# Optimization experiments

Measured on AMD Instinct MI355X. Metric: run time of the kernel, lower is better.

The kernel has to match this reference:

```python
import jax, jax.numpy as jnp
import numpy as np


def setup_inputs() -> dict:
    key = jax.random.key(0)
    ks = jax.random.split(key, 7)
    B, T, D = 4, 4096, 128
    s = 0.02
    return {
        "input_data": jax.random.normal(ks[0], (B, T, D), dtype=jnp.float32),
        "Wq": jax.random.normal(ks[1], (D, D), dtype=jnp.float32) * s,
        "bq": jax.random.normal(ks[2], (D,), dtype=jnp.float32) * s,
        "Wk": jax.random.normal(ks[3], (D, D), dtype=jnp.float32) * s,
        "bk": jax.random.normal(ks[4], (D,), dtype=jnp.float32) * s,
        "Wv": jax.random.normal(ks[5], (D, D), dtype=jnp.float32) * s,
        "bv": jax.random.normal(ks[6], (D,), dtype=jnp.float32) * s,
    }


def reference(input_data, Wq, bq, Wk, bk, Wv, bv):
    D = input_data.shape[-1]
    scale = jnp.asarray(D, input_data.dtype) ** 0.5
    # torch Linear: x @ W.T + b
    q = input_data @ Wq.T + bq  # [B,T,D]
    k = input_data @ Wk.T + bk
    v = input_data @ Wv.T + bv
    energy = jnp.einsum("btd,bsd->bts", q, k) / scale  # [B,T,T]
    attn = jax.nn.softmax(energy, axis=-1)
    return jnp.einsum("bts,bsd->btd", attn, v)  # [B,T,D]
```

## Files before the change

kernel.cpp:

```cpp
#include <hip/hip_runtime.h>
#include <cstdint>

typedef _Float16 half2_t __attribute__((ext_vector_type(2)));
typedef _Float16 half4_t __attribute__((ext_vector_type(4)));
typedef _Float16 half8_t __attribute__((ext_vector_type(8)));
typedef float floatx4 __attribute__((ext_vector_type(4)));

#define T_SEQ 4096
#define D_HEAD 128
#define SCALE_LOG2 0.12751742526f

__device__ __forceinline__ void gload16(const void* src, void* dst_lds) {
    using gptr_t = const __attribute__((address_space(1))) unsigned int*;
    using lptr_t = __attribute__((address_space(3))) unsigned int*;
    __builtin_amdgcn_global_load_lds((gptr_t)(uintptr_t)src,
                                     (lptr_t)(unsigned int)(uintptr_t)dst_lds, 16, 0, 0);
}

__device__ __forceinline__ float exp2_raw(float x) {
#if __has_builtin(__builtin_amdgcn_exp2f)
    return __builtin_amdgcn_exp2f(x);
#else
    return exp2f(x);
#endif
}

__global__ __launch_bounds__(256) void proj_kernel(
    const float* __restrict__ x,
    const float* __restrict__ Wq, const float* __restrict__ bq,
    const float* __restrict__ Wk, const float* __restrict__ bk,
    const float* __restrict__ Wv, const float* __restrict__ bv,
    _Float16* __restrict__ qf, _Float16* __restrict__ kf, _Float16* __restrict__ vt)
{
    __shared__ __align__(16) _Float16 Ws[128 * 136];
    __shared__ __align__(16) _Float16 xs[64 * 136];

    const int t = threadIdx.x;
    const int mat = blockIdx.y;
    const float* W = (mat == 0) ? Wq : (mat == 1) ? Wk : Wv;
    const float* bias = (mat == 0) ? bq : (mat == 1) ? bk : bv;
    const float osc = (mat == 0) ? SCALE_LOG2 : 1.0f;
    const int r0 = blockIdx.x * 64;

    {
        const int o = t >> 1;
        const int i0 = (t & 1) * 64;
        for (int jj = 0; jj < 8; ++jj) {
            floatx4 w0 = *reinterpret_cast<const floatx4*>(W + o * 128 + i0 + jj * 8);
            floatx4 w1 = *reinterpret_cast<const floatx4*>(W + o * 128 + i0 + jj * 8 + 4);
            half8_t h;
            h[0]=(_Float16)w0[0]; h[1]=(_Float16)w0[1]; h[2]=(_Float16)w0[2]; h[3]=(_Float16)w0[3];
            h[4]=(_Float16)w1[0]; h[5]=(_Float16)w1[1]; h[6]=(_Float16)w1[2]; h[7]=(_Float16)w1[3];
            *reinterpret_cast<half8_t*>(&Ws[o * 136 + i0 + jj * 8]) = h;
        }
    }
    {
        const int row = t >> 2;
        const int c0 = (t & 3) * 32;
        for (int jj = 0; jj < 4; ++jj) {
            floatx4 w0 = *reinterpret_cast<const floatx4*>(x + (size_t)(r0 + row) * 128 + c0 + jj * 8);
            floatx4 w1 = *reinterpret_cast<const floatx4*>(x + (size_t)(r0 + row) * 128 + c0 + jj * 8 + 4);
            half8_t h;
            h[0]=(_Float16)w0[0]; h[1]=(_Float16)w0[1]; h[2]=(_Float16)w0[2]; h[3]=(_Float16)w0[3];
            h[4]=(_Float16)w1[0]; h[5]=(_Float16)w1[1]; h[6]=(_Float16)w1[2]; h[7]=(_Float16)w1[3];
            *reinterpret_cast<half8_t*>(&xs[row * 136 + c0 + jj * 8]) = h;
        }
    }
    __syncthreads();

    const int w = t >> 6;
    const int lane = t & 63;
    const int lo = lane & 15, hi = lane >> 4;

    floatx4 acc[8] = {};
    for (int dc = 0; dc < 4; ++dc) {
        half8_t a8 = *reinterpret_cast<const half8_t*>(&xs[(w * 16 + lo) * 136 + dc * 32 + hi * 8]);
        for (int ot = 0; ot < 8; ++ot) {
            half8_t b8 = *reinterpret_cast<const half8_t*>(&Ws[(ot * 16 + lo) * 136 + dc * 32 + hi * 8]);
            acc[ot] = __builtin_amdgcn_mfma_f32_16x16x32_f16(a8, b8, acc[ot], 0, 0, 0);
        }
    }
    __syncthreads();

    float bb[8];
    for (int ot = 0; ot < 8; ++ot) bb[ot] = bias[ot * 16 + lo];

    if (mat < 2) {
        _Float16* ol = xs;
        for (int ot = 0; ot < 8; ++ot)
            for (int r = 0; r < 4; ++r)
                ol[(w * 16 + hi * 4 + r) * 136 + ot * 16 + lo] = (_Float16)((acc[ot][r] + bb[ot]) * osc);
        __syncthreads();
        _Float16* dst = (mat == 0) ? qf : kf;
        for (int i = 0; i < 4; ++i) {
            int c = t + 256 * i;
            int row = c >> 4, p = c & 15;
            half8_t v = *reinterpret_cast<const half8_t*>(&ol[row * 136 + p * 8]);
            *reinterpret_cast<half8_t*>(dst + (size_t)(r0 + row) * 128 + p * 8) = v;
        }
    } else {
        _Float16* vl = Ws;
        for (int ot = 0; ot < 8; ++ot)
            for (int r = 0; r < 4; ++r)
                vl[(ot * 16 + lo) * 72 + w * 16 + hi * 4 + r] = (_Float16)(acc[ot][r] + bb[ot]);
        __syncthreads();
        const int b = r0 >> 12, tl0 = r0 & 4095;
        for (int i = 0; i < 4; ++i) {
            int c = t + 256 * i;
            int d = c >> 3, p = c & 7;
            half8_t v = *reinterpret_cast<const half8_t*>(&vl[d * 72 + p * 8]);
            *reinterpret_cast<half8_t*>(vt + ((size_t)(b * 128 + d)) * 4096 + tl0 + p * 8) = v;
        }
    }
}

__global__ __launch_bounds__(512, 1) void attn_kernel(
    const _Float16* __restrict__ qf, const _Float16* __restrict__ kf,
    const _Float16* __restrict__ vt, float* __restrict__ out)
{
    __shared__ __align__(16) char smem[100352];

    const int tid = threadIdx.x;
    const int w = tid >> 6, lane = tid & 63;
    const int lo = lane & 15, hi = lane >> 4;
    const int qg = w & 1, ksp = w >> 1;

    const int bx = blockIdx.x;
    const int wg = (bx & 7) * 32 + (bx >> 3);
    const int b = wg >> 6;
    const int q0 = (wg & 63) * 64;

    const char* kbc = (const char*)(kf + (size_t)b * T_SEQ * 128);
    const char* vbc = (const char*)(vt + (size_t)b * 128 * T_SEQ);

    int koff[2], kdst[2];
#pragma unroll
    for (int r = 0; r < 2; ++r) {
        int seg = w * 2 + r;
        int slot = lane & 15;
        int row = seg * 4 + (lane >> 4);
        koff[r] = row * 256 + ((slot ^ (row & 7)) << 4);
        kdst[r] = seg * 1024 + lane * 16;
    }
    int vgo[2], vwl[2];
#pragma unroll
    for (int i = 0; i < 2; ++i) {
        int d = (tid >> 3) + 64 * i;
        vgo[i] = d * (T_SEQ * 2) + (tid & 7) * 16;
        vwl[i] = 16384 + d * 128 + (((tid & 7) ^ (d & 7)) << 4);
    }
    int kro[4];
#pragma unroll
    for (int dc = 0; dc < 4; ++dc)
        kro[dc] = (ksp * 16 + lo) * 256 + (((dc * 4 + hi) ^ (lo & 7)) << 4);
    int vro[8];
#pragma unroll
    for (int dt = 0; dt < 8; ++dt)
        vro[dt] = 16384 + (dt * 16 + lo) * 128 +
                  (((ksp * 2 + (hi >> 1)) ^ (lo & 7)) << 4) + ((hi & 1) << 3);

    half8_t qfA[4], qfB[4];
    {
        const _Float16* qa = qf + ((size_t)b * T_SEQ + q0 + qg * 32 + lo) * 128;
        const _Float16* qb = qa + 16 * 128;
#pragma unroll
        for (int dc = 0; dc < 4; ++dc) {
            qfA[dc] = *reinterpret_cast<const half8_t*>(qa + dc * 32 + hi * 8);
            qfB[dc] = *reinterpret_cast<const half8_t*>(qb + dc * 32 + hi * 8);
        }
    }

    floatx4 accA[8] = {}, accB[8] = {};
    float mA = -1e30f, mB = -1e30f, lA = 0.f, lB = 0.f;
    half4_t paA = {}, paB = {};

    gload16(kbc + koff[0], smem + kdst[0]);
    gload16(kbc + koff[1], smem + kdst[1]);
    {
        uint4 v0 = *reinterpret_cast<const uint4*>(vbc + vgo[0]);
        uint4 v1 = *reinterpret_cast<const uint4*>(vbc + vgo[1]);
        *reinterpret_cast<uint4*>(smem + vwl[0]) = v0;
        *reinterpret_cast<uint4*>(smem + vwl[1]) = v1;
    }
    __syncthreads();

#define TILE(T0, CUR, NXT, PRV, PF, DOPREV) do {                                       \
    uint4 vr0, vr1;                                                                    \
    if (PF) {                                                                          \
        const char* vs = vbc + (size_t)((T0) + 64) * 2;                                \
        vr0 = *reinterpret_cast<const uint4*>(vs + vgo[0]);                            \
        vr1 = *reinterpret_cast<const uint4*>(vs + vgo[1]);                            \
        const char* ks = kbc + (size_t)((T0) + 64) * 256;                              \
        gload16(ks + koff[0], smem + (NXT) + kdst[0]);                                 \
        gload16(ks + koff[1], smem + (NXT) + kdst[1]);                                 \
    }                                                                                  \
    floatx4 sA = {0.f,0.f,0.f,0.f}, sB = {0.f,0.f,0.f,0.f};                            \
    __builtin_amdgcn_s_setprio(1);                                                     \
    _Pragma("unroll")                                                                  \
    for (int dc = 0; dc < 4; ++dc) {                                                   \
        half8_t kf8 = *reinterpret_cast<const half8_t*>(smem + (CUR) + kro[dc]);       \
        sA = __builtin_amdgcn_mfma_f32_16x16x32_f16(kf8, qfA[dc], sA, 0, 0, 0);        \
        sB = __builtin_amdgcn_mfma_f32_16x16x32_f16(kf8, qfB[dc], sB, 0, 0, 0);        \
    }                                                                                  \
    __builtin_amdgcn_s_setprio(0);                                                     \
    float mpA = fmaxf(fmaxf(sA[0], sA[1]), fmaxf(sA[2], sA[3]));                       \
    float mpB = fmaxf(fmaxf(sB[0], sB[1]), fmaxf(sB[2], sB[3]));                       \
    bool ok = (mpA <= mA + 4.0f) && (mpB <= mB + 4.0f);                                \
    if (!__all(ok)) {                                                                  \
        float ra = mpA, rb = mpB;                                                      \
        ra = fmaxf(ra, __shfl_xor(ra, 16)); ra = fmaxf(ra, __shfl_xor(ra, 32));        \
        rb = fmaxf(rb, __shfl_xor(rb, 16)); rb = fmaxf(rb, __shfl_xor(rb, 32));        \
        float nA = fmaxf(mA, ra), nB = fmaxf(mB, rb);                                  \
        float aA = exp2_raw(mA - nA), aB = exp2_raw(mB - nB);                          \
        lA *= aA; lB *= aB;                                                            \
        _Pragma("unroll")                                                              \
        for (int dt = 0; dt < 8; ++dt) { accA[dt] *= aA; accB[dt] *= aB; }             \
        mA = nA; mB = nB;                                                              \
    }                                                                                  \
    if (DOPREV) {                                                                      \
        __builtin_amdgcn_s_setprio(1);                                                 \
        _Pragma("unroll")                                                              \
        for (int dt = 0; dt < 8; ++dt) {                                               \
            half4_t vfr = *reinterpret_cast<const half4_t*>(smem + (PRV) + vro[dt]);   \
            accA[dt] = __builtin_amdgcn_mfma_f32_16x16x16f16(vfr, paA, accA[dt], 0, 0, 0); \
            accB[dt] = __builtin_amdgcn_mfma_f32_16x16x16f16(vfr, paB, accB[dt], 0, 0, 0); \
        }                                                                              \
        __builtin_amdgcn_s_setprio(0);                                                 \
    }                                                                                  \
    {                                                                                  \
        float p0 = exp2_raw(sA[0] - mA), p1 = exp2_raw(sA[1] - mA);                    \
        float p2 = exp2_raw(sA[2] - mA), p3 = exp2_raw(sA[3] - mA);                    \
        lA += (p0 + p1) + (p2 + p3);                                                   \
        half2_t h0 = __builtin_bit_cast(half2_t, __builtin_amdgcn_cvt_pkrtz(p0, p1));  \
        half2_t h1 = __builtin_bit_cast(half2_t, __builtin_amdgcn_cvt_pkrtz(p2, p3));  \
        paA[0] = h0[0]; paA[1] = h0[1]; paA[2] = h1[0]; paA[3] = h1[1];                \
        p0 = exp2_raw(sB[0] - mB); p1 = exp2_raw(sB[1] - mB);                          \
        p2 = exp2_raw(sB[2] - mB); p3 = exp2_raw(sB[3] - mB);                          \
        lB += (p0 + p1) + (p2 + p3);                                                   \
        h0 = __builtin_bit_cast(half2_t, __builtin_amdgcn_cvt_pkrtz(p0, p1));          \
        h1 = __builtin_bit_cast(half2_t, __builtin_amdgcn_cvt_pkrtz(p2, p3));          \
        paB[0] = h0[0]; paB[1] = h0[1]; paB[2] = h1[0]; paB[3] = h1[1];                \
    }                                                                                  \
    if (PF) {                                                                          \
        *reinterpret_cast<uint4*>(smem + (NXT) + vwl[0]) = vr0;                        \
        *reinterpret_cast<uint4*>(smem + (NXT) + vwl[1]) = vr1;                        \
    }                                                                                  \
    __syncthreads();                                                                   \
} while (0)

    TILE(0, 0, 32768, 65536, 1, 0);
    for (int t0 = 1; t0 < 61; t0 += 3) {
        TILE(t0 * 64,       32768, 65536, 0,     1, 1);
        TILE(t0 * 64 + 64,  65536, 0,     32768, 1, 1);
        TILE(t0 * 64 + 128, 0,     32768, 65536, 1, 1);
    }
    TILE(61 * 64, 32768, 65536, 0,     1, 1);
    TILE(62 * 64, 65536, 0,     32768, 1, 1);
    TILE(63 * 64, 0,     32768, 65536, 0, 1);
#undef TILE

#pragma unroll
    for (int dt = 0; dt < 8; ++dt) {
        half4_t vfr = *reinterpret_cast<const half4_t*>(smem + 0 + vro[dt]);
        accA[dt] = __builtin_amdgcn_mfma_f32_16x16x16f16(vfr, paA, accA[dt], 0, 0, 0);
        accB[dt] = __builtin_amdgcn_mfma_f32_16x16x16f16(vfr, paB, accB[dt], 0, 0, 0);
    }

    lA += __shfl_xor(lA, 16); lA += __shfl_xor(lA, 32);
    lB += __shfl_xor(lB, 16); lB += __shfl_xor(lB, 32);

    float* red_m = reinterpret_cast<float*>(smem + 98304);
    float* red_l = reinterpret_cast<float*>(smem + 99328);
    const int rowA = qg * 32 + lo, rowB = qg * 32 + 16 + lo;
    if (hi == 0) {
        red_m[ksp * 64 + rowA] = mA; red_l[ksp * 64 + rowA] = lA;
        red_m[ksp * 64 + rowB] = mB; red_l[ksp * 64 + rowB] = lB;
    }
    __syncthreads();
    float facA, facB;
    {
        float M = -1e30f, L = 0.f;
#pragma unroll
        for (int s = 0; s < 4; ++s) M = fmaxf(M, red_m[s * 64 + rowA]);
#pragma unroll
        for (int s = 0; s < 4; ++s) L += red_l[s * 64 + rowA] * exp2_raw(red_m[s * 64 + rowA] - M);
        facA = exp2_raw(mA - M) / L;
        M = -1e30f; L = 0.f;
#pragma unroll
        for (int s = 0; s < 4; ++s) M = fmaxf(M, red_m[s * 64 + rowB]);
#pragma unroll
        for (int s = 0; s < 4; ++s) L += red_l[s * 64 + rowB] * exp2_raw(red_m[s * 64 + rowB] - M);
        facB = exp2_raw(mB - M) / L;
    }
    float* out_lds = reinterpret_cast<float*>(smem);
    for (int s = 0; s < 4; ++s) {
        if (ksp == s) {
#pragma unroll
            for (int dt = 0; dt < 8; ++dt)
#pragma unroll
                for (int r = 0; r < 4; ++r) {
                    int d = dt * 16 + hi * 4 + r;
                    float vA = accA[dt][r] * facA;
                    float vB = accB[dt][r] * facB;
                    float* pA = &out_lds[rowA * 132 + d];
                    float* pB = &out_lds[rowB * 132 + d];
                    if (s == 0) { *pA = vA; *pB = vB; }
                    else        { *pA += vA; *pB += vB; }
                }
        }
        __syncthreads();
    }
    {
        int row = tid >> 3, d0 = (tid & 7) * 16;
        float* op = out + ((size_t)b * T_SEQ + q0 + row) * 128 + d0;
#pragma unroll
        for (int j = 0; j < 4; ++j) {
            float4 v;
            v.x = out_lds[row * 132 + d0 + j * 4 + 0];
            v.y = out_lds[row * 132 + d0 + j * 4 + 1];
            v.z = out_lds[row * 132 + d0 + j * 4 + 2];
            v.w = out_lds[row * 132 + d0 + j * 4 + 3];
            *reinterpret_cast<float4*>(op + j * 4) = v;
        }
    }
}

extern "C" void kernel_launch(void* const* d_in, const int* in_sizes, int n_in,
                              void* d_out, int out_size, void* d_ws, size_t ws_size,
                              hipStream_t stream)
{
    (void)in_sizes; (void)n_in; (void)out_size; (void)ws_size;
    const float* x  = (const float*)d_in[0];
    const float* Wq = (const float*)d_in[1];
    const float* bq = (const float*)d_in[2];
    const float* Wk = (const float*)d_in[3];
    const float* bk = (const float*)d_in[4];
    const float* Wv = (const float*)d_in[5];
    const float* bv = (const float*)d_in[6];
    float* out = (float*)d_out;

    _Float16* qf = (_Float16*)d_ws;
    _Float16* kf = qf + (size_t)4 * T_SEQ * D_HEAD;
    _Float16* vt = kf + (size_t)4 * T_SEQ * D_HEAD;

    proj_kernel<<<dim3(256, 3), 256, 0, stream>>>(x, Wq, bq, Wk, bk, Wv, bv, qf, kf, vt);
    attn_kernel<<<dim3(256), 512, 0, stream>>>(qf, kf, vt, out);
}
```

Before: 78.41 us.

## Load V fragments directly from global into registers, bypassing LDS staging

V tiles are no longer staged through shared memory. Each lane now loads its half4 MFMA operand fragments straight from global memory into two register buffers that alternate between tiles. The K pipeline shrinks from triple to double buffering, cutting LDS from about 98KB to 36KB. This removes LDS writes and reads for V, at the cost of more registers and narrower, strided 8-byte global loads that may coalesce less well.

Measured after the change: 180.6 us. 130% more time.

```diff
diff --git a/kernel.cpp b/kernel.cpp
--- a/kernel.cpp
+++ b/kernel.cpp
@@ -118,7 +118,7 @@
     const _Float16* __restrict__ qf, const _Float16* __restrict__ kf,
     const _Float16* __restrict__ vt, float* __restrict__ out)
 {
-    __shared__ __align__(16) char smem[100352];
+    __shared__ __align__(16) char smem[36864];
 
     const int tid = threadIdx.x;
     const int w = tid >> 6, lane = tid & 63;
@@ -142,22 +142,12 @@
         koff[r] = row * 256 + ((slot ^ (row & 7)) << 4);
         kdst[r] = seg * 1024 + lane * 16;
     }
-    int vgo[2], vwl[2];
-#pragma unroll
-    for (int i = 0; i < 2; ++i) {
-        int d = (tid >> 3) + 64 * i;
-        vgo[i] = d * (T_SEQ * 2) + (tid & 7) * 16;
-        vwl[i] = 16384 + d * 128 + (((tid & 7) ^ (d & 7)) << 4);
-    }
     int kro[4];
 #pragma unroll
     for (int dc = 0; dc < 4; ++dc)
         kro[dc] = (ksp * 16 + lo) * 256 + (((dc * 4 + hi) ^ (lo & 7)) << 4);
-    int vro[8];
-#pragma unroll
-    for (int dt = 0; dt < 8; ++dt)
-        vro[dt] = 16384 + (dt * 16 + lo) * 128 +
-                  (((ksp * 2 + (hi >> 1)) ^ (lo & 7)) << 4) + ((hi & 1) << 3);
+
+    const int vgo = lo * 8192 + ksp * 32 + hi * 8;
 
     half8_t qfA[4], qfB[4];
     {
@@ -173,23 +163,17 @@
     floatx4 accA[8] = {}, accB[8] = {};
     float mA = -1e30f, mB = -1e30f, lA = 0.f, lB = 0.f;
     half4_t paA = {}, paB = {};
+    half4_t v0[8], v1[8];
 
     gload16(kbc + koff[0], smem + kdst[0]);
     gload16(kbc + koff[1], smem + kdst[1]);
-    {
-        uint4 v0 = *reinterpret_cast<const uint4*>(vbc + vgo[0]);
-        uint4 v1 = *reinterpret_cast<const uint4*>(vbc + vgo[1]);
-        *reinterpret_cast<uint4*>(smem + vwl[0]) = v0;
-        *reinterpret_cast<uint4*>(smem + vwl[1]) = v1;
-    }
+#pragma unroll
+    for (int dt = 0; dt < 8; ++dt)
+        v0[dt] = *reinterpret_cast<const half4_t*>(vbc + vgo + dt * 131072);
     __syncthreads();
 
-#define TILE(T0, CUR, NXT, PRV, PF, DOPREV) do {                                       \
-    uint4 vr0, vr1;                                                                    \
+#define TILE(T0, CUR, NXT, VOTH, PF, DOPREV) do {                                      \
     if (PF) {                                                                          \
-        const char* vs = vbc + (size_t)((T0) + 64) * 2;                                \
-        vr0 = *reinterpret_cast<const uint4*>(vs + vgo[0]);                            \
-        vr1 = *reinterpret_cast<const uint4*>(vs + vgo[1]);                            \
         const char* ks = kbc + (size_t)((T0) + 64) * 256;                              \
         gload16(ks + koff[0], smem + (NXT) + kdst[0]);                                 \
         gload16(ks + koff[1], smem + (NXT) + kdst[1]);                                 \
@@ -221,11 +205,16 @@
         __builtin_amdgcn_s_setprio(1);                                                 \
         _Pragma("unroll")                                                              \
         for (int dt = 0; dt < 8; ++dt) {                                               \
-            half4_t vfr = *reinterpret_cast<const half4_t*>(smem + (PRV) + vro[dt]);   \
-            accA[dt] = __builtin_amdgcn_mfma_f32_16x16x16f16(vfr, paA, accA[dt], 0, 0, 0); \
-            accB[dt] = __builtin_amdgcn_mfma_f32_16x16x16f16(vfr, paB, accB[dt], 0, 0, 0); \
+            accA[dt] = __builtin_amdgcn_mfma_f32_16x16x16f16(VOTH[dt], paA, accA[dt], 0, 0, 0); \
+            accB[dt] = __builtin_amdgcn_mfma_f32_16x16x16f16(VOTH[dt], paB, accB[dt], 0, 0, 0); \
         }                                                                              \
         __builtin_amdgcn_s_setprio(0);                                                 \
+    }                                                                                  \
+    if (PF) {                                                                          \
+        const char* vs = vbc + (size_t)((T0) + 64) * 2 + vgo;                          \
+        _Pragma("unroll")                                                              \
+        for (int dt = 0; dt < 8; ++dt)                                                 \
+            VOTH[dt] = *reinterpret_cast<const half4_t*>(vs + dt * 131072);            \
     }                                                                                  \
     {                                                                                  \
         float p0 = exp2_raw(sA[0] - mA), p1 = exp2_raw(sA[1] - mA);                    \
@@ -241,36 +230,28 @@
         h1 = __builtin_bit_cast(half2_t, __builtin_amdgcn_cvt_pkrtz(p2, p3));          \
         paB[0] = h0[0]; paB[1] = h0[1]; paB[2] = h1[0]; paB[3] = h1[1];                \
     }                                                                                  \
-    if (PF) {                                                                          \
-        *reinterpret_cast<uint4*>(smem + (NXT) + vwl[0]) = vr0;                        \
-        *reinterpret_cast<uint4*>(smem + (NXT) + vwl[1]) = vr1;                        \
-    }                                                                                  \
     __syncthreads();                                                                   \
 } while (0)
 
-    TILE(0, 0, 32768, 65536, 1, 0);
-    for (int t0 = 1; t0 < 61; t0 += 3) {
-        TILE(t0 * 64,       32768, 65536, 0,     1, 1);
-        TILE(t0 * 64 + 64,  65536, 0,     32768, 1, 1);
-        TILE(t0 * 64 + 128, 0,     32768, 65536, 1, 1);
-    }
-    TILE(61 * 64, 32768, 65536, 0,     1, 1);
-    TILE(62 * 64, 65536, 0,     32768, 1, 1);
-    TILE(63 * 64, 0,     32768, 65536, 0, 1);
+    TILE(0, 0, 16384, v1, 1, 0);
+    for (int tt = 64; tt < 3968; tt += 128) {
+        TILE(tt,      16384, 0,     v0, 1, 1);
+        TILE(tt + 64, 0,     16384, v1, 1, 1);
+    }
+    TILE(4032, 16384, 0, v0, 0, 1);
 #undef TILE
 
 #pragma unroll
     for (int dt = 0; dt < 8; ++dt) {
-        half4_t vfr = *reinterpret_cast<const half4_t*>(smem + 0 + vro[dt]);
-        accA[dt] = __builtin_amdgcn_mfma_f32_16x16x16f16(vfr, paA, accA[dt], 0, 0, 0);
-        accB[dt] = __builtin_amdgcn_mfma_f32_16x16x16f16(vfr, paB, accB[dt], 0, 0, 0);
+        accA[dt] = __builtin_amdgcn_mfma_f32_16x16x16f16(v1[dt], paA, accA[dt], 0, 0, 0);
+        accB[dt] = __builtin_amdgcn_mfma_f32_16x16x16f16(v1[dt], paB, accB[dt], 0, 0, 0);
     }
 
     lA += __shfl_xor(lA, 16); lA += __shfl_xor(lA, 32);
     lB += __shfl_xor(lB, 16); lB += __shfl_xor(lB, 32);
 
-    float* red_m = reinterpret_cast<float*>(smem + 98304);
-    float* red_l = reinterpret_cast<float*>(smem + 99328);
+    float* red_m = reinterpret_cast<float*>(smem + 34816);
+    float* red_l = reinterpret_cast<float*>(smem + 35840);
     const int rowA = qg * 32 + lo, rowB = qg * 32 + 16 + lo;
     if (hi == 0) {
         red_m[ksp * 64 + rowA] = mA; red_l[ksp * 64 + rowA] = lA;
```
